# Optimization experiments

Hardware: AMD Instinct MI355X
Metric: run time of the kernel (lower is better)

The kernel has to match this reference:

```python
import jax, jax.numpy as jnp
import numpy as np

N_NODES = 50000
N_EDGES = 800000
N_GRAPHS = 64
NEG_SLOPE = 0.2  # PyG GATConv default LeakyReLU slope


def _gat_layer(x, src, dst, W, a_src, a_dst, bias, n_nodes):
    """Single-head GATConv: gather -> segment-softmax over dst -> scatter-add."""
    h = x @ W                                   # [N, F]
    e = jax.nn.leaky_relu(
        (h @ a_src)[src] + (h @ a_dst)[dst], NEG_SLOPE)  # [E]
    # numerically-stable segment softmax over incoming edges of each dst node
    m = jax.ops.segment_max(e, dst, num_segments=n_nodes)   # [N]
    e = jnp.exp(e - m[dst])
    s = jax.ops.segment_sum(e, dst, num_segments=n_nodes)   # [N]
    alpha = e / s[dst]                                       # [E]
    out = jax.ops.segment_sum(alpha[:, None] * h[src], dst, num_segments=n_nodes)
    return out + bias


def setup_inputs() -> dict:
    key = jax.random.key(0)
    ks = jax.random.split(key, 16)
    x = jax.random.normal(ks[0], (N_NODES, 3), dtype=jnp.float32)
    edge_index = jax.random.randint(ks[1], (2, N_EDGES), 0, N_NODES, dtype=jnp.int64)
    edge_attr = jax.random.normal(ks[2], (N_EDGES, 4), dtype=jnp.float32)
    batch = jnp.sort(jax.random.randint(ks[3], (N_NODES,), 0, N_GRAPHS, dtype=jnp.int64))

    def glorot(k, shape):
        lim = float(np.sqrt(6.0 / (shape[0] + shape[-1])))
        return jax.random.uniform(k, shape, jnp.float32, -lim, lim)

    return {
        "x": x, "edge_index": edge_index, "edge_attr": edge_attr, "batch": batch,
        "W1": glorot(ks[4], (3, 8)),
        "a_src1": glorot(ks[5], (8,)),
        "a_dst1": glorot(ks[6], (8,)),
        "b1": jnp.zeros((8,), jnp.float32),
        "W2": glorot(ks[7], (8, 256)),
        "a_src2": glorot(ks[8], (256,)),
        "a_dst2": glorot(ks[9], (256,)),
        "b2": jnp.zeros((256,), jnp.float32),
        "fc_w": glorot(ks[10], (256, 1)),
        "fc_b": jnp.zeros((1,), jnp.float32),
    }


def reference(x, edge_index, edge_attr, batch,
              W1, a_src1, a_dst1, b1, W2, a_src2, a_dst2, b2, fc_w, fc_b):
    n = x.shape[0]
    loops = jnp.arange(n, dtype=edge_index.dtype)
    src = jnp.concatenate([edge_index[0], loops])  # add_self_loops=True
    dst = jnp.concatenate([edge_index[1], loops])
    # edge_attr is unused by GATConv when edge_dim=None (PyG default)
    h = jax.nn.relu(_gat_layer(x, src, dst, W1, a_src1, a_dst1, b1, n))
    h = jax.nn.relu(_gat_layer(h, src, dst, W2, a_src2, a_dst2, b2, n))
    h = h @ fc_w + fc_b                               # [N, 1]
    out = jax.ops.segment_sum(h, batch, num_segments=N_GRAPHS)  # global_add_pool
    return out
```

## Files before the change

kernel.cpp:

```cpp
#include <hip/hip_runtime.h>
#include <math.h>

static constexpr int NN = 50000;
static constexpr int NE = 800000;
static constexpr int NG = 64;
static constexpr int CAP = 64;
static constexpr float SLOPE = 0.2f;
static constexpr int NGRP = (NN + 15) / 16;

__global__ void __launch_bounds__(256) k_init_all(
    const float* __restrict__ x, const float* __restrict__ W1,
    const float* __restrict__ a1s, const float* __restrict__ a1d,
    const int* __restrict__ ei,
    const float* __restrict__ W2, const float* __restrict__ a2s,
    const float* __restrict__ a2d,
    float* __restrict__ h1, float* __restrict__ hs1, float* __restrict__ hd1,
    int* __restrict__ counts, int* __restrict__ ell,
    float* __restrict__ w2sd, float* __restrict__ out) {
  if (blockIdx.x == 0) {
    if (threadIdx.x < NG) out[threadIdx.x] = 0.f;
    int w = threadIdx.x >> 6, lane = threadIdx.x & 63;
    for (int tt = w * 4; tt < w * 4 + 4; ++tt) {
      int k = tt >> 1, sel = tt & 1;
      const float* a = sel ? a2d : a2s;
      float acc = 0.f;
      for (int j = lane; j < 256; j += 64) acc += W2[256 * k + j] * a[j];
      for (int off = 32; off; off >>= 1) acc += __shfl_down(acc, off);
      if (lane == 0) w2sd[tt] = acc;
    }
  }
  int stride = gridDim.x * 256;
  for (int t = blockIdx.x * 256 + threadIdx.x; t < NE; t += stride) {
    if (t < NN) {
      float x0 = x[3*t], x1 = x[3*t+1], x2 = x[3*t+2];
      float hs = 0.f, hd = 0.f;
      float v[8];
#pragma unroll
      for (int f = 0; f < 8; ++f) {
        v[f] = x0 * W1[f] + x1 * W1[8+f] + x2 * W1[16+f];
        hs += v[f] * a1s[f];
        hd += v[f] * a1d[f];
      }
      float4* h4 = reinterpret_cast<float4*>(h1 + 8*t);
      h4[0] = make_float4(v[0], v[1], v[2], v[3]);
      h4[1] = make_float4(v[4], v[5], v[6], v[7]);
      hs1[t] = hs; hd1[t] = hd;
    }
    int s = ei[t];
    int d = ei[NE + t];
    int r = atomicAdd(&counts[d], 1);
    if (r < CAP) ell[d * CAP + r] = s;
  }
}

__device__ __forceinline__ void gather16(int n, int l, int deg,
                                         const int* __restrict__ row,
                                         const float* __restrict__ hs,
                                         const float* __restrict__ hd,
                                         const float* __restrict__ feat,
                                         float acc[8]) {
  float hdn = hd[n];
  float s = 0.f;
#pragma unroll
  for (int f = 0; f < 8; ++f) acc[f] = 0.f;
  for (int j = l - 1; j < deg; j += 16) {
    int src = (j < 0) ? n : row[j];
    float el = hs[src] + hdn;
    el = el >= 0.f ? el : SLOPE * el;
    float w = __expf(el);
    s += w;
    const float4* f4 = reinterpret_cast<const float4*>(feat + 8*src);
    float4 lo = f4[0], hi = f4[1];
    acc[0] += w*lo.x; acc[1] += w*lo.y; acc[2] += w*lo.z; acc[3] += w*lo.w;
    acc[4] += w*hi.x; acc[5] += w*hi.y; acc[6] += w*hi.z; acc[7] += w*hi.w;
  }
#pragma unroll
  for (int off = 8; off; off >>= 1) {
    s += __shfl_xor(s, off, 16);
#pragma unroll
    for (int f = 0; f < 8; ++f) acc[f] += __shfl_xor(acc[f], off, 16);
  }
  float inv = 1.f / s;
#pragma unroll
  for (int f = 0; f < 8; ++f) acc[f] *= inv;
}

__global__ void __launch_bounds__(256) k_layer1(
    const int* __restrict__ counts, const int* __restrict__ ell,
    const float* __restrict__ h1, const float* __restrict__ hs1,
    const float* __restrict__ hd1, const float* __restrict__ b1,
    const float* __restrict__ w2sd,
    float* __restrict__ out1, float* __restrict__ hs2, float* __restrict__ hd2) {
  int sub = threadIdx.x >> 4, l = threadIdx.x & 15;
  for (int gb = blockIdx.x; gb < NGRP; gb += gridDim.x) {
    int n = gb * 16 + sub;
    if (n >= NN) continue;
    int deg = min(counts[n], CAP);
    float acc[8];
    gather16(n, l, deg, ell + n * CAP, hs1, hd1, h1, acc);
    if (l == 0) {
      float hs = 0.f, hd = 0.f;
      float v[8];
#pragma unroll
      for (int f = 0; f < 8; ++f) {
        v[f] = fmaxf(acc[f] + b1[f], 0.f);
        hs += v[f] * w2sd[2*f];
        hd += v[f] * w2sd[2*f+1];
      }
      float4* o4 = reinterpret_cast<float4*>(out1 + 8*n);
      o4[0] = make_float4(v[0], v[1], v[2], v[3]);
      o4[1] = make_float4(v[4], v[5], v[6], v[7]);
      hs2[n] = hs; hd2[n] = hd;
    }
  }
}

__global__ void __launch_bounds__(256) k_layer2final(
    const int* __restrict__ counts, const int* __restrict__ ell,
    const float* __restrict__ out1, const float* __restrict__ hs2,
    const float* __restrict__ hd2, const float* __restrict__ b2,
    const float* __restrict__ W2, const float* __restrict__ fcw,
    const float* __restrict__ fcb, const int* __restrict__ batch,
    float* __restrict__ out) {
  __shared__ float sW2[2048];
  __shared__ float sb2[256];
  __shared__ float sfc[256];
  __shared__ float bins[NG];
  for (int i = threadIdx.x; i < 2048; i += 256) sW2[i] = W2[i];
  sb2[threadIdx.x] = b2[threadIdx.x];
  sfc[threadIdx.x] = fcw[threadIdx.x];
  if (threadIdx.x < NG) bins[threadIdx.x] = 0.f;
  __syncthreads();

  int sub = threadIdx.x >> 4, l = threadIdx.x & 15;
  float fcb0 = fcb[0];
  for (int gb = blockIdx.x; gb < NGRP; gb += gridDim.x) {
    int n = gb * 16 + sub;
    if (n >= NN) continue;
    int deg = min(counts[n], CAP);
    float acc[8];
    gather16(n, l, deg, ell + n * CAP, hs2, hd2, out1, acc);
    float y = 0.f;
    for (int i = 0; i < 16; ++i) {
      int j = l + 16 * i;
      float o = sb2[j];
#pragma unroll
      for (int k = 0; k < 8; ++k) o += acc[k] * sW2[256*k + j];
      o = fmaxf(o, 0.f);
      y += o * sfc[j];
    }
#pragma unroll
    for (int off = 8; off; off >>= 1) y += __shfl_xor(y, off, 16);
    if (l == 0) atomicAdd(&bins[batch[n]], y + fcb0);
  }
  __syncthreads();
  if (threadIdx.x < NG) {
    float v = bins[threadIdx.x];
    if (v != 0.f) atomicAdd(&out[threadIdx.x], v);
  }
}

extern "C" void kernel_launch(void* const* d_in, const int* in_sizes, int n_in,
                              void* d_out, int out_size, void* d_ws, size_t ws_size,
                              hipStream_t stream) {
  const float* x    = (const float*)d_in[0];
  const int*   ei   = (const int*)d_in[1];
  const int*   batch= (const int*)d_in[3];
  const float* W1   = (const float*)d_in[4];
  const float* a1s  = (const float*)d_in[5];
  const float* a1d  = (const float*)d_in[6];
  const float* b1   = (const float*)d_in[7];
  const float* W2   = (const float*)d_in[8];
  const float* a2s  = (const float*)d_in[9];
  const float* a2d  = (const float*)d_in[10];
  const float* b2   = (const float*)d_in[11];
  const float* fcw  = (const float*)d_in[12];
  const float* fcb  = (const float*)d_in[13];
  float* out = (float*)d_out;

  float* ws   = (float*)d_ws;
  float* h1   = ws;
  float* out1 = h1   + 400000;
  float* hs1  = out1 + 400000;
  float* hd1  = hs1  + 50000;
  float* hs2  = hd1  + 50000;
  float* hd2  = hs2  + 50000;
  float* w2sd = hd2  + 50000;
  int* counts = (int*)(w2sd + 16);
  int* ell    = counts + 50000;

  hipMemsetAsync(counts, 0, NN * sizeof(int), stream);

  k_init_all<<<2048, 256, 0, stream>>>(x, W1, a1s, a1d, ei, W2, a2s, a2d,
                                       h1, hs1, hd1, counts, ell, w2sd, out);
  k_layer1<<<1024, 256, 0, stream>>>(counts, ell, h1, hs1, hd1, b1, w2sd,
                                     out1, hs2, hd2);
  k_layer2final<<<1024, 256, 0, stream>>>(counts, ell, out1, hs2, hd2, b2,
                                          W2, fcw, fcb, batch, out);
}
```

Measured before the change: 193.2 us.

## Fuse three kernels into one persistent kernel with grid-wide barriers

Merges the init/CSR-build, layer-1 and layer-2+pooling kernels into a single persistent kernel of 512 blocks, separated by atomic-counter grid barriers. Barrier counters are cleared by the existing memset. The aim is to remove two kernel launches and their inter-kernel gaps. In exchange, the grid shrinks for the edge-scatter phase, the kernel depends on all 512 blocks being co-resident to avoid deadlock, and it adds spin-wait barrier latency.

```diff
diff --git a/kernel.cpp b/kernel.cpp
--- a/kernel.cpp
+++ b/kernel.cpp
@@ -7,50 +7,17 @@
 static constexpr int CAP = 64;
 static constexpr float SLOPE = 0.2f;
 static constexpr int NGRP = (NN + 15) / 16;
-
-__global__ void __launch_bounds__(256) k_init_all(
-    const float* __restrict__ x, const float* __restrict__ W1,
-    const float* __restrict__ a1s, const float* __restrict__ a1d,
-    const int* __restrict__ ei,
-    const float* __restrict__ W2, const float* __restrict__ a2s,
-    const float* __restrict__ a2d,
-    float* __restrict__ h1, float* __restrict__ hs1, float* __restrict__ hd1,
-    int* __restrict__ counts, int* __restrict__ ell,
-    float* __restrict__ w2sd, float* __restrict__ out) {
-  if (blockIdx.x == 0) {
-    if (threadIdx.x < NG) out[threadIdx.x] = 0.f;
-    int w = threadIdx.x >> 6, lane = threadIdx.x & 63;
-    for (int tt = w * 4; tt < w * 4 + 4; ++tt) {
-      int k = tt >> 1, sel = tt & 1;
-      const float* a = sel ? a2d : a2s;
-      float acc = 0.f;
-      for (int j = lane; j < 256; j += 64) acc += W2[256 * k + j] * a[j];
-      for (int off = 32; off; off >>= 1) acc += __shfl_down(acc, off);
-      if (lane == 0) w2sd[tt] = acc;
-    }
-  }
-  int stride = gridDim.x * 256;
-  for (int t = blockIdx.x * 256 + threadIdx.x; t < NE; t += stride) {
-    if (t < NN) {
-      float x0 = x[3*t], x1 = x[3*t+1], x2 = x[3*t+2];
-      float hs = 0.f, hd = 0.f;
-      float v[8];
-#pragma unroll
-      for (int f = 0; f < 8; ++f) {
-        v[f] = x0 * W1[f] + x1 * W1[8+f] + x2 * W1[16+f];
-        hs += v[f] * a1s[f];
-        hd += v[f] * a1d[f];
-      }
-      float4* h4 = reinterpret_cast<float4*>(h1 + 8*t);
-      h4[0] = make_float4(v[0], v[1], v[2], v[3]);
-      h4[1] = make_float4(v[4], v[5], v[6], v[7]);
-      hs1[t] = hs; hd1[t] = hd;
-    }
-    int s = ei[t];
-    int d = ei[NE + t];
-    int r = atomicAdd(&counts[d], 1);
-    if (r < CAP) ell[d * CAP + r] = s;
-  }
+static constexpr int GRID = 512;
+
+__device__ __forceinline__ void gbar(unsigned* bar, int phase, unsigned nblk) {
+  __syncthreads();
+  if (threadIdx.x == 0) {
+    __threadfence();
+    atomicAdd(&bar[phase], 1u);
+    while (atomicAdd(&bar[phase], 0u) < nblk) __builtin_amdgcn_s_sleep(32);
+    __threadfence();
+  }
+  __syncthreads();
 }
 
 __device__ __forceinline__ void gather16(int n, int l, int deg,
@@ -85,14 +52,62 @@
   for (int f = 0; f < 8; ++f) acc[f] *= inv;
 }
 
-__global__ void __launch_bounds__(256) k_layer1(
-    const int* __restrict__ counts, const int* __restrict__ ell,
-    const float* __restrict__ h1, const float* __restrict__ hs1,
-    const float* __restrict__ hd1, const float* __restrict__ b1,
-    const float* __restrict__ w2sd,
-    float* __restrict__ out1, float* __restrict__ hs2, float* __restrict__ hd2) {
+__global__ void __launch_bounds__(256, 2) k_fused(
+    const float* __restrict__ x, const int* __restrict__ ei,
+    const int* __restrict__ batch,
+    const float* __restrict__ W1, const float* __restrict__ a1s,
+    const float* __restrict__ a1d, const float* __restrict__ b1,
+    const float* __restrict__ W2, const float* __restrict__ a2s,
+    const float* __restrict__ a2d, const float* __restrict__ b2,
+    const float* __restrict__ fcw, const float* __restrict__ fcb,
+    float* __restrict__ h1, float* __restrict__ out1,
+    float* __restrict__ hs1, float* __restrict__ hd1,
+    float* __restrict__ hs2, float* __restrict__ hd2,
+    float* __restrict__ w2sd, int* __restrict__ counts,
+    unsigned* __restrict__ bar, int* __restrict__ ell,
+    float* __restrict__ out) {
+  __shared__ float sW2[2048];
+  __shared__ float sb2[256];
+  __shared__ float sfc[256];
+  __shared__ float bins[NG];
+
+  if (blockIdx.x == 0) {
+    if (threadIdx.x < NG) out[threadIdx.x] = 0.f;
+    int w = threadIdx.x >> 6, lane = threadIdx.x & 63;
+    for (int tt = w * 4; tt < w * 4 + 4; ++tt) {
+      int k = tt >> 1, sel = tt & 1;
+      const float* a = sel ? a2d : a2s;
+      float acc = 0.f;
+      for (int j = lane; j < 256; j += 64) acc += W2[256 * k + j] * a[j];
+      for (int off = 32; off; off >>= 1) acc += __shfl_down(acc, off);
+      if (lane == 0) w2sd[tt] = acc;
+    }
+  }
+  for (int t = blockIdx.x * 256 + threadIdx.x; t < NE; t += GRID * 256) {
+    if (t < NN) {
+      float x0 = x[3*t], x1 = x[3*t+1], x2 = x[3*t+2];
+      float hs = 0.f, hd = 0.f;
+      float v[8];
+#pragma unroll
+      for (int f = 0; f < 8; ++f) {
+        v[f] = x0 * W1[f] + x1 * W1[8+f] + x2 * W1[16+f];
+        hs += v[f] * a1s[f];
+        hd += v[f] * a1d[f];
+      }
+      float4* h4 = reinterpret_cast<float4*>(h1 + 8*t);
+      h4[0] = make_float4(v[0], v[1], v[2], v[3]);
+      h4[1] = make_float4(v[4], v[5], v[6], v[7]);
+      hs1[t] = hs; hd1[t] = hd;
+    }
+    int s = ei[t];
+    int d = ei[NE + t];
+    int r = atomicAdd(&counts[d], 1);
+    if (r < CAP) ell[d * CAP + r] = s;
+  }
+  gbar(bar, 0, GRID);
+
   int sub = threadIdx.x >> 4, l = threadIdx.x & 15;
-  for (int gb = blockIdx.x; gb < NGRP; gb += gridDim.x) {
+  for (int gb = blockIdx.x; gb < NGRP; gb += GRID) {
     int n = gb * 16 + sub;
     if (n >= NN) continue;
     int deg = min(counts[n], CAP);
@@ -113,28 +128,16 @@
       hs2[n] = hs; hd2[n] = hd;
     }
   }
-}
-
-__global__ void __launch_bounds__(256) k_layer2final(
-    const int* __restrict__ counts, const int* __restrict__ ell,
-    const float* __restrict__ out1, const float* __restrict__ hs2,
-    const float* __restrict__ hd2, const float* __restrict__ b2,
-    const float* __restrict__ W2, const float* __restrict__ fcw,
-    const float* __restrict__ fcb, const int* __restrict__ batch,
-    float* __restrict__ out) {
-  __shared__ float sW2[2048];
-  __shared__ float sb2[256];
-  __shared__ float sfc[256];
-  __shared__ float bins[NG];
+  gbar(bar, 1, GRID);
+
   for (int i = threadIdx.x; i < 2048; i += 256) sW2[i] = W2[i];
   sb2[threadIdx.x] = b2[threadIdx.x];
   sfc[threadIdx.x] = fcw[threadIdx.x];
   if (threadIdx.x < NG) bins[threadIdx.x] = 0.f;
   __syncthreads();
 
-  int sub = threadIdx.x >> 4, l = threadIdx.x & 15;
   float fcb0 = fcb[0];
-  for (int gb = blockIdx.x; gb < NGRP; gb += gridDim.x) {
+  for (int gb = blockIdx.x; gb < NGRP; gb += GRID) {
     int n = gb * 16 + sub;
     if (n >= NN) continue;
     int deg = min(counts[n], CAP);
@@ -187,14 +190,13 @@
   float* hd2  = hs2  + 50000;
   float* w2sd = hd2  + 50000;
   int* counts = (int*)(w2sd + 16);
-  int* ell    = counts + 50000;
-
-  hipMemsetAsync(counts, 0, NN * sizeof(int), stream);
-
-  k_init_all<<<2048, 256, 0, stream>>>(x, W1, a1s, a1d, ei, W2, a2s, a2d,
-                                       h1, hs1, hd1, counts, ell, w2sd, out);
-  k_layer1<<<1024, 256, 0, stream>>>(counts, ell, h1, hs1, hd1, b1, w2sd,
-                                     out1, hs2, hd2);
-  k_layer2final<<<1024, 256, 0, stream>>>(counts, ell, out1, hs2, hd2, b2,
-                                          W2, fcw, fcb, batch, out);
-}
+  unsigned* bar = (unsigned*)(counts + 50000);
+  int* ell    = (int*)(bar + 2);
+
+  hipMemsetAsync(counts, 0, (50000 + 2) * sizeof(int), stream);
+
+  k_fused<<<GRID, 256, 0, stream>>>(x, ei, batch, W1, a1s, a1d, b1,
+                                    W2, a2s, a2d, b2, fcw, fcb,
+                                    h1, out1, hs1, hd1, hs2, hd2,
+                                    w2sd, counts, bar, ell, out);
+}
```

Measured after the change: 302.8 us. +56.7%, slower.
